# Kernel tuning notes

Hardware: AMD Instinct MI355X
Metric: run time of the kernel (lower is better)

## Reference

```python
import jax, jax.numpy as jnp
import numpy as np

# Fixed genome topology (layered DAG, topologically ordered levels)
B = 4096      # batch
N_IN = 512    # input nodes
H1 = 1536     # hidden level 1
H2 = 1536     # hidden level 2
N_OUT = 512   # output nodes
FAN = 32      # fan-in per non-input node


def setup_inputs() -> dict:
    key = jax.random.key(0)
    ks = jax.random.split(key, 10)
    x = jax.random.normal(ks[0], (B, N_IN), dtype=jnp.float32)
    # level 1: sources among inputs [0, N_IN)
    src0 = jax.random.randint(ks[1], (H1 * FAN,), 0, N_IN, dtype=jnp.int32)
    dst0 = jax.random.randint(ks[2], (H1 * FAN,), 0, H1, dtype=jnp.int32)
    w0 = jax.random.normal(ks[3], (H1 * FAN,), dtype=jnp.float32) * 0.1
    # level 2: sources among inputs + level1 [0, N_IN+H1)
    src1 = jax.random.randint(ks[4], (H2 * FAN,), 0, N_IN + H1, dtype=jnp.int32)
    dst1 = jax.random.randint(ks[5], (H2 * FAN,), 0, H2, dtype=jnp.int32)
    w1 = jax.random.normal(ks[6], (H2 * FAN,), dtype=jnp.float32) * 0.1
    # output level: sources among all earlier nodes [0, N_IN+H1+H2)
    src2 = jax.random.randint(ks[7], (N_OUT * FAN,), 0, N_IN + H1 + H2, dtype=jnp.int32)
    dst2 = jax.random.randint(ks[8], (N_OUT * FAN,), 0, N_OUT, dtype=jnp.int32)
    w2 = jax.random.normal(ks[9], (N_OUT * FAN,), dtype=jnp.float32) * 0.1
    return dict(x=x, src0=src0, dst0=dst0, w0=w0,
                src1=src1, dst1=dst1, w1=w1,
                src2=src2, dst2=dst2, w2=w2)


def _level(node_values, src, dst, w, size):
    # per-edge weighted gather: [B, E]
    vals = node_values[:, src] * w
    # scatter-add into destination nodes of this level: [B, size]
    agg = jnp.zeros((node_values.shape[0], size), node_values.dtype).at[:, dst].add(vals)
    # per-node activation (genome.activation == 'relu'); relu(0)=0 matches
    # original's behavior of leaving unconnected nodes at zero
    return jax.nn.relu(agg)


def reference(x, src0, dst0, w0, src1, dst1, w1, src2, dst2, w2):
    nv = x                                        # [B, N_IN]
    h1 = _level(nv, src0, dst0, w0, H1)           # [B, H1]
    nv = jnp.concatenate([nv, h1], axis=1)        # [B, N_IN+H1]
    h2 = _level(nv, src1, dst1, w1, H2)           # [B, H2]
    nv = jnp.concatenate([nv, h2], axis=1)        # [B, N_IN+H1+H2]
    out = _level(nv, src2, dst2, w2, N_OUT)       # [B, N_OUT]
    return out
```

## Files before the change

### kernel.cpp

```cpp
#include <hip/hip_runtime.h>
#include <hip/hip_fp16.h>
#include <stdint.h>

#define BATCH 4096
#define N_IN  512
#define H1    1536
#define H2    1536
#define N_OUT 512
#define FAN   32
#define E0 (H1 * FAN)
#define E1 (H2 * FAN)
#define E2 (N_OUT * FAN)
#define ETOT (E0 + E1 + E2)
#define NNODES (H1 + H2 + N_OUT)
#define MAXDEG 128

#define OFF_EDGES 33554432
#define OFF_CNT   (OFF_EDGES + NNODES * MAXDEG * 8)

__global__ __launch_bounds__(256) void k_transpose_in(const float* __restrict__ x,
                                                      __half* __restrict__ xT) {
    __shared__ float tile[32][33];
    const int tx = threadIdx.x, ty = threadIdx.y;
    const int n0 = blockIdx.x * 32;
    const int b0 = blockIdx.y * 32;
#pragma unroll
    for (int k = 0; k < 32; k += 8)
        tile[ty + k][tx] = x[(size_t)(b0 + ty + k) * N_IN + (n0 + tx)];
    __syncthreads();
#pragma unroll
    for (int k = 0; k < 32; k += 8)
        xT[(size_t)(n0 + ty + k) * BATCH + (b0 + tx)] = __float2half_rn(tile[tx][ty + k]);
}

__global__ __launch_bounds__(256) void k_fill(const int* __restrict__ s0, const int* __restrict__ d0, const float* __restrict__ w0,
                                              const int* __restrict__ s1, const int* __restrict__ d1, const float* __restrict__ w1,
                                              const int* __restrict__ s2, const int* __restrict__ d2, const float* __restrict__ w2,
                                              int* __restrict__ cnt, int2* __restrict__ edges) {
    const int e = blockIdx.x * 256 + threadIdx.x;
    int src, node; float w;
    if (e < E0)           { src = s0[e];          node = d0[e];                w = w0[e]; }
    else if (e < E0 + E1) { int i = e - E0;       src = s1[i]; node = H1 + d1[i];        w = w1[i]; }
    else                  { int i = e - E0 - E1;  src = s2[i]; node = H1 + H2 + d2[i];   w = w2[i]; }
    const int pos = atomicAdd(&cnt[node], 1);
    if (pos < MAXDEG) edges[node * MAXDEG + pos] = make_int2(src, __float_as_int(w));
}

__global__ __launch_bounds__(256, 8)
void k_level(const int2* __restrict__ edges,
             const int* __restrict__ cnt,
             const uint4* __restrict__ nv,
             uint4* __restrict__ outb) {
    const int lane = threadIdx.x & 63;
    const int wv   = threadIdx.x >> 6;
    const int node = __builtin_amdgcn_readfirstlane((blockIdx.y << 2) | wv);
    const int col8 = (blockIdx.x << 6) | lane;

    int c = cnt[node];
    c = (c < 0) ? 0 : (c > MAXDEG ? MAXDEG : c);

    float a0 = 0.f, a1 = 0.f, a2 = 0.f, a3 = 0.f, a4 = 0.f, a5 = 0.f, a6 = 0.f, a7 = 0.f;

#define ACC8(q, W) {                                                    \
    const __half2 h0 = *(const __half2*)&(q).x;                         \
    const __half2 h1 = *(const __half2*)&(q).y;                         \
    const __half2 h2 = *(const __half2*)&(q).z;                         \
    const __half2 h3 = *(const __half2*)&(q).w;                         \
    a0 = fmaf(__low2float(h0),  (W), a0);                               \
    a1 = fmaf(__high2float(h0), (W), a1);                               \
    a2 = fmaf(__low2float(h1),  (W), a2);                               \
    a3 = fmaf(__high2float(h1), (W), a3);                               \
    a4 = fmaf(__low2float(h2),  (W), a4);                               \
    a5 = fmaf(__high2float(h2), (W), a5);                               \
    a6 = fmaf(__low2float(h3),  (W), a6);                               \
    a7 = fmaf(__high2float(h3), (W), a7); }

    for (int base = 0; base < c; base += 64) {
        const int2 my = edges[(size_t)node * MAXDEG + base + lane];
        const int m = (c - base < 64) ? (c - base) : 64;
        int j = 0;
        for (; j + 4 <= m; j += 4) {
            const int   s0i = __builtin_amdgcn_readlane(my.x, j)     & 4095;
            const int   s1i = __builtin_amdgcn_readlane(my.x, j + 1) & 4095;
            const int   s2i = __builtin_amdgcn_readlane(my.x, j + 2) & 4095;
            const int   s3i = __builtin_amdgcn_readlane(my.x, j + 3) & 4095;
            const float wa  = __int_as_float(__builtin_amdgcn_readlane(my.y, j));
            const float wb  = __int_as_float(__builtin_amdgcn_readlane(my.y, j + 1));
            const float wc  = __int_as_float(__builtin_amdgcn_readlane(my.y, j + 2));
            const float wd  = __int_as_float(__builtin_amdgcn_readlane(my.y, j + 3));
            const uint4 q0 = nv[((size_t)s0i << 9) | col8];
            const uint4 q1 = nv[((size_t)s1i << 9) | col8];
            const uint4 q2 = nv[((size_t)s2i << 9) | col8];
            const uint4 q3 = nv[((size_t)s3i << 9) | col8];
            ACC8(q0, wa);
            ACC8(q1, wb);
            ACC8(q2, wc);
            ACC8(q3, wd);
        }
        for (; j < m; ++j) {
            const int   s0i = __builtin_amdgcn_readlane(my.x, j) & 4095;
            const float wa  = __int_as_float(__builtin_amdgcn_readlane(my.y, j));
            const uint4 q0 = nv[((size_t)s0i << 9) | col8];
            ACC8(q0, wa);
        }
    }
#undef ACC8

    a0 = fmaxf(a0, 0.f); a1 = fmaxf(a1, 0.f); a2 = fmaxf(a2, 0.f); a3 = fmaxf(a3, 0.f);
    a4 = fmaxf(a4, 0.f); a5 = fmaxf(a5, 0.f); a6 = fmaxf(a6, 0.f); a7 = fmaxf(a7, 0.f);

    const __half2 h0 = __floats2half2_rn(a0, a1);
    const __half2 h1 = __floats2half2_rn(a2, a3);
    const __half2 h2 = __floats2half2_rn(a4, a5);
    const __half2 h3 = __floats2half2_rn(a6, a7);
    uint4 p;
    p.x = *(const uint32_t*)&h0; p.y = *(const uint32_t*)&h1;
    p.z = *(const uint32_t*)&h2; p.w = *(const uint32_t*)&h3;
    outb[((size_t)node << 9) | col8] = p;
}

__global__ __launch_bounds__(256) void k_transpose_out(const __half* __restrict__ outh,
                                                       float* __restrict__ out) {
    __shared__ float tile[32][33];
    const int tx = threadIdx.x, ty = threadIdx.y;
    const int n0 = blockIdx.x * 32;
    const int b0 = blockIdx.y * 32;
#pragma unroll
    for (int k = 0; k < 32; k += 8)
        tile[ty + k][tx] = __half2float(outh[(size_t)(n0 + ty + k) * BATCH + (b0 + tx)]);
    __syncthreads();
#pragma unroll
    for (int k = 0; k < 32; k += 8)
        out[(size_t)(b0 + ty + k) * N_OUT + (n0 + tx)] = tile[tx][ty + k];
}

extern "C" void kernel_launch(void* const* d_in, const int* in_sizes, int n_in,
                              void* d_out, int out_size, void* d_ws, size_t ws_size,
                              hipStream_t stream) {
    const float* x  = (const float*)d_in[0];
    const int* s0   = (const int*)d_in[1];
    const int* dd0  = (const int*)d_in[2];
    const float* w0 = (const float*)d_in[3];
    const int* s1   = (const int*)d_in[4];
    const int* dd1  = (const int*)d_in[5];
    const float* w1 = (const float*)d_in[6];
    const int* s2   = (const int*)d_in[7];
    const int* dd2  = (const int*)d_in[8];
    const float* w2 = (const float*)d_in[9];

    char* ws        = (char*)d_ws;
    uint4*    nv4   = (uint4*)ws;
    int2*     edges = (int2*)(ws + OFF_EDGES);
    int*      cnt   = (int*)(ws + OFF_CNT);

    hipMemsetAsync(cnt, 0, NNODES * sizeof(int), stream);
    k_fill<<<ETOT / 256, 256, 0, stream>>>(s0, dd0, w0, s1, dd1, w1, s2, dd2, w2, cnt, edges);

    k_transpose_in<<<dim3(N_IN / 32, BATCH / 32), dim3(32, 8), 0, stream>>>(x, (__half*)ws);

    k_level<<<dim3(8, H1 / 4), 256, 0, stream>>>(edges, cnt, nv4,
                                                 nv4 + (size_t)N_IN * 512);
    k_level<<<dim3(8, H2 / 4), 256, 0, stream>>>(edges + (size_t)H1 * MAXDEG, cnt + H1, nv4,
                                                 nv4 + (size_t)(N_IN + H1) * 512);
    k_level<<<dim3(8, N_OUT / 4), 256, 0, stream>>>(edges + (size_t)(H1 + H2) * MAXDEG, cnt + H1 + H2, nv4,
                                                    nv4 + (size_t)(N_IN + H1 + H2) * 512);

    k_transpose_out<<<dim3(N_OUT / 32, BATCH / 32), dim3(32, 8), 0, stream>>>(
        (const __half*)(ws + (size_t)(N_IN + H1 + H2) * BATCH * 2), (float*)d_out);
}
```

Measured before the change: 147.6 us.

## Split batch columns into two launches per level with 8-byte gathers

Each level kernel now handles 4 fp16 batch columns per lane with uint2 loads instead of 8 with uint4, and is launched twice per level over the two halves of the batch. Each launch touches a smaller slice of node values, so its working set is halved and may fit better in cache, and each thread holds fewer accumulators. In exchange there are twice as many launches, the edge lists and counts are read twice, and per-lane loads are narrower, which can lower achieved memory bandwidth.

```diff
diff --git a/kernel.cpp b/kernel.cpp
--- a/kernel.cpp
+++ b/kernel.cpp
@@ -49,31 +49,26 @@
 __global__ __launch_bounds__(256, 8)
 void k_level(const int2* __restrict__ edges,
              const int* __restrict__ cnt,
-             const uint4* __restrict__ nv,
-             uint4* __restrict__ outb) {
+             const uint2* __restrict__ nv,
+             uint2* __restrict__ outb,
+             const int cb4) {
     const int lane = threadIdx.x & 63;
     const int wv   = threadIdx.x >> 6;
     const int node = __builtin_amdgcn_readfirstlane((blockIdx.y << 2) | wv);
-    const int col8 = (blockIdx.x << 6) | lane;
+    const int col4 = cb4 + (blockIdx.x << 6) + lane;
 
     int c = cnt[node];
     c = (c < 0) ? 0 : (c > MAXDEG ? MAXDEG : c);
 
-    float a0 = 0.f, a1 = 0.f, a2 = 0.f, a3 = 0.f, a4 = 0.f, a5 = 0.f, a6 = 0.f, a7 = 0.f;
+    float a0 = 0.f, a1 = 0.f, a2 = 0.f, a3 = 0.f;
 
-#define ACC8(q, W) {                                                    \
+#define ACC4(q, W) {                                                    \
     const __half2 h0 = *(const __half2*)&(q).x;                         \
     const __half2 h1 = *(const __half2*)&(q).y;                         \
-    const __half2 h2 = *(const __half2*)&(q).z;                         \
-    const __half2 h3 = *(const __half2*)&(q).w;                         \
     a0 = fmaf(__low2float(h0),  (W), a0);                               \
     a1 = fmaf(__high2float(h0), (W), a1);                               \
     a2 = fmaf(__low2float(h1),  (W), a2);                               \
-    a3 = fmaf(__high2float(h1), (W), a3);                               \
-    a4 = fmaf(__low2float(h2),  (W), a4);                               \
-    a5 = fmaf(__high2float(h2), (W), a5);                               \
-    a6 = fmaf(__low2float(h3),  (W), a6);                               \
-    a7 = fmaf(__high2float(h3), (W), a7); }
+    a3 = fmaf(__high2float(h1), (W), a3); }
 
     for (int base = 0; base < c; base += 64) {
         const int2 my = edges[(size_t)node * MAXDEG + base + lane];
@@ -88,35 +83,31 @@
             const float wb  = __int_as_float(__builtin_amdgcn_readlane(my.y, j + 1));
             const float wc  = __int_as_float(__builtin_amdgcn_readlane(my.y, j + 2));
             const float wd  = __int_as_float(__builtin_amdgcn_readlane(my.y, j + 3));
-            const uint4 q0 = nv[((size_t)s0i << 9) | col8];
-            const uint4 q1 = nv[((size_t)s1i << 9) | col8];
-            const uint4 q2 = nv[((size_t)s2i << 9) | col8];
-            const uint4 q3 = nv[((size_t)s3i << 9) | col8];
-            ACC8(q0, wa);
-            ACC8(q1, wb);
-            ACC8(q2, wc);
-            ACC8(q3, wd);
+            const uint2 q0 = nv[((size_t)s0i << 10) | col4];
+            const uint2 q1 = nv[((size_t)s1i << 10) | col4];
+            const uint2 q2 = nv[((size_t)s2i << 10) | col4];
+            const uint2 q3 = nv[((size_t)s3i << 10) | col4];
+            ACC4(q0, wa);
+            ACC4(q1, wb);
+            ACC4(q2, wc);
+            ACC4(q3, wd);
         }
         for (; j < m; ++j) {
             const int   s0i = __builtin_amdgcn_readlane(my.x, j) & 4095;
             const float wa  = __int_as_float(__builtin_amdgcn_readlane(my.y, j));
-            const uint4 q0 = nv[((size_t)s0i << 9) | col8];
-            ACC8(q0, wa);
+            const uint2 q0 = nv[((size_t)s0i << 10) | col4];
+            ACC4(q0, wa);
         }
     }
-#undef ACC8
+#undef ACC4
 
     a0 = fmaxf(a0, 0.f); a1 = fmaxf(a1, 0.f); a2 = fmaxf(a2, 0.f); a3 = fmaxf(a3, 0.f);
-    a4 = fmaxf(a4, 0.f); a5 = fmaxf(a5, 0.f); a6 = fmaxf(a6, 0.f); a7 = fmaxf(a7, 0.f);
 
     const __half2 h0 = __floats2half2_rn(a0, a1);
     const __half2 h1 = __floats2half2_rn(a2, a3);
-    const __half2 h2 = __floats2half2_rn(a4, a5);
-    const __half2 h3 = __floats2half2_rn(a6, a7);
-    uint4 p;
+    uint2 p;
     p.x = *(const uint32_t*)&h0; p.y = *(const uint32_t*)&h1;
-    p.z = *(const uint32_t*)&h2; p.w = *(const uint32_t*)&h3;
-    outb[((size_t)node << 9) | col8] = p;
+    outb[((size_t)node << 10) | col4] = p;
 }
 
 __global__ __launch_bounds__(256) void k_transpose_out(const __half* __restrict__ outh,
@@ -149,7 +140,7 @@
     const float* w2 = (const float*)d_in[9];
 
     char* ws        = (char*)d_ws;
-    uint4*    nv4   = (uint4*)ws;
+    uint2*    nv2   = (uint2*)ws;
     int2*     edges = (int2*)(ws + OFF_EDGES);
     int*      cnt   = (int*)(ws + OFF_CNT);
 
@@ -158,12 +149,18 @@
 
     k_transpose_in<<<dim3(N_IN / 32, BATCH / 32), dim3(32, 8), 0, stream>>>(x, (__half*)ws);
 
-    k_level<<<dim3(8, H1 / 4), 256, 0, stream>>>(edges, cnt, nv4,
-                                                 nv4 + (size_t)N_IN * 512);
-    k_level<<<dim3(8, H2 / 4), 256, 0, stream>>>(edges + (size_t)H1 * MAXDEG, cnt + H1, nv4,
-                                                 nv4 + (size_t)(N_IN + H1) * 512);
-    k_level<<<dim3(8, N_OUT / 4), 256, 0, stream>>>(edges + (size_t)(H1 + H2) * MAXDEG, cnt + H1 + H2, nv4,
-                                                    nv4 + (size_t)(N_IN + H1 + H2) * 512);
+    for (int cb4 = 0; cb4 <= 512; cb4 += 512) {
+        k_level<<<dim3(8, H1 / 4), 256, 0, stream>>>(edges, cnt, nv2,
+                                                     nv2 + (size_t)N_IN * 1024, cb4);
+    }
+    for (int cb4 = 0; cb4 <= 512; cb4 += 512) {
+        k_level<<<dim3(8, H2 / 4), 256, 0, stream>>>(edges + (size_t)H1 * MAXDEG, cnt + H1, nv2,
+                                                     nv2 + (size_t)(N_IN + H1) * 1024, cb4);
+    }
+    for (int cb4 = 0; cb4 <= 512; cb4 += 512) {
+        k_level<<<dim3(8, N_OUT / 4), 256, 0, stream>>>(edges + (size_t)(H1 + H2) * MAXDEG, cnt + H1 + H2, nv2,
+                                                        nv2 + (size_t)(N_IN + H1 + H2) * 1024, cb4);
+    }
 
     k_transpose_out<<<dim3(N_OUT / 32, BATCH / 32), dim3(32, 8), 0, stream>>>(
         (const __half*)(ws + (size_t)(N_IN + H1 + H2) * BATCH * 2), (float*)d_out);
```

Result: slower. 175.5 us (+18.9%).

## Fuse all stages into one cooperative persistent kernel with grid syncs

Applied to the files above, without the earlier changes.

Replaces the memset, edge fill, input transpose, three level kernels and output transpose with a single cooperative kernel of 512 blocks that separates the phases with grid-wide syncs. The goal is to remove the cost of launching multiple kernels and the gaps between them. In exchange, each level is processed by a fixed grid that loops over node groups, so there is less parallelism per level, and every phase boundary now pays for a grid barrier.

```diff
diff --git a/kernel.cpp b/kernel.cpp
--- a/kernel.cpp
+++ b/kernel.cpp
@@ -1,6 +1,9 @@
 #include <hip/hip_runtime.h>
 #include <hip/hip_fp16.h>
+#include <hip/hip_cooperative_groups.h>
 #include <stdint.h>
+
+namespace cg = cooperative_groups;
 
 #define BATCH 4096
 #define N_IN  512
@@ -15,51 +18,29 @@
 #define NNODES (H1 + H2 + N_OUT)
 #define MAXDEG 128
 
+#define NBLK   512
+#define NTHR   256
+#define GSTRIDE (NBLK * NTHR)
+
 #define OFF_EDGES 33554432
 #define OFF_CNT   (OFF_EDGES + NNODES * MAXDEG * 8)
 
-__global__ __launch_bounds__(256) void k_transpose_in(const float* __restrict__ x,
-                                                      __half* __restrict__ xT) {
-    __shared__ float tile[32][33];
-    const int tx = threadIdx.x, ty = threadIdx.y;
-    const int n0 = blockIdx.x * 32;
-    const int b0 = blockIdx.y * 32;
-#pragma unroll
-    for (int k = 0; k < 32; k += 8)
-        tile[ty + k][tx] = x[(size_t)(b0 + ty + k) * N_IN + (n0 + tx)];
-    __syncthreads();
-#pragma unroll
-    for (int k = 0; k < 32; k += 8)
-        xT[(size_t)(n0 + ty + k) * BATCH + (b0 + tx)] = __float2half_rn(tile[tx][ty + k]);
-}
-
-__global__ __launch_bounds__(256) void k_fill(const int* __restrict__ s0, const int* __restrict__ d0, const float* __restrict__ w0,
-                                              const int* __restrict__ s1, const int* __restrict__ d1, const float* __restrict__ w1,
-                                              const int* __restrict__ s2, const int* __restrict__ d2, const float* __restrict__ w2,
-                                              int* __restrict__ cnt, int2* __restrict__ edges) {
-    const int e = blockIdx.x * 256 + threadIdx.x;
-    int src, node; float w;
-    if (e < E0)           { src = s0[e];          node = d0[e];                w = w0[e]; }
-    else if (e < E0 + E1) { int i = e - E0;       src = s1[i]; node = H1 + d1[i];        w = w1[i]; }
-    else                  { int i = e - E0 - E1;  src = s2[i]; node = H1 + H2 + d2[i];   w = w2[i]; }
-    const int pos = atomicAdd(&cnt[node], 1);
-    if (pos < MAXDEG) edges[node * MAXDEG + pos] = make_int2(src, __float_as_int(w));
-}
-
-__global__ __launch_bounds__(256, 8)
-void k_level(const int2* __restrict__ edges,
-             const int* __restrict__ cnt,
-             const uint4* __restrict__ nv,
-             uint4* __restrict__ outb) {
-    const int lane = threadIdx.x & 63;
-    const int wv   = threadIdx.x >> 6;
-    const int node = __builtin_amdgcn_readfirstlane((blockIdx.y << 2) | wv);
-    const int col8 = (blockIdx.x << 6) | lane;
-
-    int c = cnt[node];
-    c = (c < 0) ? 0 : (c > MAXDEG ? MAXDEG : c);
-
-    float a0 = 0.f, a1 = 0.f, a2 = 0.f, a3 = 0.f, a4 = 0.f, a5 = 0.f, a6 = 0.f, a7 = 0.f;
+__device__ __forceinline__ void level_body(const int2* __restrict__ edges,
+                                           const int* __restrict__ cnt,
+                                           const uint4* __restrict__ nv,
+                                           uint4* __restrict__ outb,
+                                           const int H, const int b, const int tid) {
+    const int lane = tid & 63;
+    const int wv   = tid >> 6;
+    const int col8 = ((b & 7) << 6) | lane;
+    const int slot = ((b >> 3) << 2) | wv;
+
+    for (int n0 = 0; n0 < H; n0 += 256) {
+        const int node = __builtin_amdgcn_readfirstlane(n0 + slot);
+        int c = cnt[node];
+        c = (c < 0) ? 0 : (c > MAXDEG ? MAXDEG : c);
+
+        float a0 = 0.f, a1 = 0.f, a2 = 0.f, a3 = 0.f, a4 = 0.f, a5 = 0.f, a6 = 0.f, a7 = 0.f;
 
 #define ACC8(q, W) {                                                    \
     const __half2 h0 = *(const __half2*)&(q).x;                         \
@@ -75,63 +56,122 @@
     a6 = fmaf(__low2float(h3),  (W), a6);                               \
     a7 = fmaf(__high2float(h3), (W), a7); }
 
-    for (int base = 0; base < c; base += 64) {
-        const int2 my = edges[(size_t)node * MAXDEG + base + lane];
-        const int m = (c - base < 64) ? (c - base) : 64;
-        int j = 0;
-        for (; j + 4 <= m; j += 4) {
-            const int   s0i = __builtin_amdgcn_readlane(my.x, j)     & 4095;
-            const int   s1i = __builtin_amdgcn_readlane(my.x, j + 1) & 4095;
-            const int   s2i = __builtin_amdgcn_readlane(my.x, j + 2) & 4095;
-            const int   s3i = __builtin_amdgcn_readlane(my.x, j + 3) & 4095;
-            const float wa  = __int_as_float(__builtin_amdgcn_readlane(my.y, j));
-            const float wb  = __int_as_float(__builtin_amdgcn_readlane(my.y, j + 1));
-            const float wc  = __int_as_float(__builtin_amdgcn_readlane(my.y, j + 2));
-            const float wd  = __int_as_float(__builtin_amdgcn_readlane(my.y, j + 3));
-            const uint4 q0 = nv[((size_t)s0i << 9) | col8];
-            const uint4 q1 = nv[((size_t)s1i << 9) | col8];
-            const uint4 q2 = nv[((size_t)s2i << 9) | col8];
-            const uint4 q3 = nv[((size_t)s3i << 9) | col8];
-            ACC8(q0, wa);
-            ACC8(q1, wb);
-            ACC8(q2, wc);
-            ACC8(q3, wd);
+        for (int base = 0; base < c; base += 64) {
+            const int2 my = edges[(size_t)node * MAXDEG + base + lane];
+            const int m = (c - base < 64) ? (c - base) : 64;
+            int j = 0;
+            for (; j + 4 <= m; j += 4) {
+                const int   s0i = __builtin_amdgcn_readlane(my.x, j)     & 4095;
+                const int   s1i = __builtin_amdgcn_readlane(my.x, j + 1) & 4095;
+                const int   s2i = __builtin_amdgcn_readlane(my.x, j + 2) & 4095;
+                const int   s3i = __builtin_amdgcn_readlane(my.x, j + 3) & 4095;
+                const float wa  = __int_as_float(__builtin_amdgcn_readlane(my.y, j));
+                const float wb  = __int_as_float(__builtin_amdgcn_readlane(my.y, j + 1));
+                const float wc  = __int_as_float(__builtin_amdgcn_readlane(my.y, j + 2));
+                const float wd  = __int_as_float(__builtin_amdgcn_readlane(my.y, j + 3));
+                const uint4 q0 = nv[((size_t)s0i << 9) | col8];
+                const uint4 q1 = nv[((size_t)s1i << 9) | col8];
+                const uint4 q2 = nv[((size_t)s2i << 9) | col8];
+                const uint4 q3 = nv[((size_t)s3i << 9) | col8];
+                ACC8(q0, wa);
+                ACC8(q1, wb);
+                ACC8(q2, wc);
+                ACC8(q3, wd);
+            }
+            for (; j < m; ++j) {
+                const int   s0i = __builtin_amdgcn_readlane(my.x, j) & 4095;
+                const float wa  = __int_as_float(__builtin_amdgcn_readlane(my.y, j));
+                const uint4 q0 = nv[((size_t)s0i << 9) | col8];
+                ACC8(q0, wa);
+            }
         }
-        for (; j < m; ++j) {
-            const int   s0i = __builtin_amdgcn_readlane(my.x, j) & 4095;
-            const float wa  = __int_as_float(__builtin_amdgcn_readlane(my.y, j));
-            const uint4 q0 = nv[((size_t)s0i << 9) | col8];
-            ACC8(q0, wa);
+#undef ACC8
+
+        a0 = fmaxf(a0, 0.f); a1 = fmaxf(a1, 0.f); a2 = fmaxf(a2, 0.f); a3 = fmaxf(a3, 0.f);
+        a4 = fmaxf(a4, 0.f); a5 = fmaxf(a5, 0.f); a6 = fmaxf(a6, 0.f); a7 = fmaxf(a7, 0.f);
+
+        const __half2 h0 = __floats2half2_rn(a0, a1);
+        const __half2 h1 = __floats2half2_rn(a2, a3);
+        const __half2 h2 = __floats2half2_rn(a4, a5);
+        const __half2 h3 = __floats2half2_rn(a6, a7);
+        uint4 p;
+        p.x = *(const uint32_t*)&h0; p.y = *(const uint32_t*)&h1;
+        p.z = *(const uint32_t*)&h2; p.w = *(const uint32_t*)&h3;
+        outb[((size_t)node << 9) | col8] = p;
+    }
+}
+
+__global__ __launch_bounds__(NTHR, 8)
+void k_mega(const float* __restrict__ x,
+            const int* __restrict__ s0, const int* __restrict__ d0, const float* __restrict__ w0,
+            const int* __restrict__ s1, const int* __restrict__ d1, const float* __restrict__ w1,
+            const int* __restrict__ s2, const int* __restrict__ d2, const float* __restrict__ w2,
+            uint4* __restrict__ nv4, int2* __restrict__ edges, int* __restrict__ cnt,
+            float* __restrict__ out) {
+    cg::grid_group grid = cg::this_grid();
+    const int tid = threadIdx.x;
+    const int b   = blockIdx.x;
+
+    __shared__ float tile[32][33];
+
+    for (int i = b * NTHR + tid; i < NNODES; i += GSTRIDE) cnt[i] = 0;
+    grid.sync();
+
+    for (int e = b * NTHR + tid; e < ETOT; e += GSTRIDE) {
+        int src, node; float w;
+        if (e < E0)           { src = s0[e];          node = d0[e];              w = w0[e]; }
+        else if (e < E0 + E1) { int i = e - E0;       src = s1[i]; node = H1 + d1[i];      w = w1[i]; }
+        else                  { int i = e - E0 - E1;  src = s2[i]; node = H1 + H2 + d2[i]; w = w2[i]; }
+        const int pos = atomicAdd(&cnt[node], 1);
+        if (pos < MAXDEG) edges[node * MAXDEG + pos] = make_int2(src, __float_as_int(w));
+    }
+
+    {
+        __half* xT = (__half*)nv4;
+        const int tx = tid & 31, ty = tid >> 5;
+        for (int i = 0; i < 4; ++i) {
+            const int t  = b * 4 + i;
+            const int n0 = (t & 15) << 5;
+            const int b0 = (t >> 4) << 5;
+            __syncthreads();
+#pragma unroll
+            for (int k = 0; k < 32; k += 8)
+                tile[ty + k][tx] = x[(size_t)(b0 + ty + k) * N_IN + (n0 + tx)];
+            __syncthreads();
+#pragma unroll
+            for (int k = 0; k < 32; k += 8)
+                xT[(size_t)(n0 + ty + k) * BATCH + (b0 + tx)] = __float2half_rn(tile[tx][ty + k]);
         }
     }
-#undef ACC8
-
-    a0 = fmaxf(a0, 0.f); a1 = fmaxf(a1, 0.f); a2 = fmaxf(a2, 0.f); a3 = fmaxf(a3, 0.f);
-    a4 = fmaxf(a4, 0.f); a5 = fmaxf(a5, 0.f); a6 = fmaxf(a6, 0.f); a7 = fmaxf(a7, 0.f);
-
-    const __half2 h0 = __floats2half2_rn(a0, a1);
-    const __half2 h1 = __floats2half2_rn(a2, a3);
-    const __half2 h2 = __floats2half2_rn(a4, a5);
-    const __half2 h3 = __floats2half2_rn(a6, a7);
-    uint4 p;
-    p.x = *(const uint32_t*)&h0; p.y = *(const uint32_t*)&h1;
-    p.z = *(const uint32_t*)&h2; p.w = *(const uint32_t*)&h3;
-    outb[((size_t)node << 9) | col8] = p;
-}
-
-__global__ __launch_bounds__(256) void k_transpose_out(const __half* __restrict__ outh,
-                                                       float* __restrict__ out) {
-    __shared__ float tile[32][33];
-    const int tx = threadIdx.x, ty = threadIdx.y;
-    const int n0 = blockIdx.x * 32;
-    const int b0 = blockIdx.y * 32;
-#pragma unroll
-    for (int k = 0; k < 32; k += 8)
-        tile[ty + k][tx] = __half2float(outh[(size_t)(n0 + ty + k) * BATCH + (b0 + tx)]);
-    __syncthreads();
-#pragma unroll
-    for (int k = 0; k < 32; k += 8)
-        out[(size_t)(b0 + ty + k) * N_OUT + (n0 + tx)] = tile[tx][ty + k];
+    grid.sync();
+
+    level_body(edges, cnt, nv4,
+               nv4 + (size_t)N_IN * 512, H1, b, tid);
+    grid.sync();
+    level_body(edges + (size_t)H1 * MAXDEG, cnt + H1, nv4,
+               nv4 + (size_t)(N_IN + H1) * 512, H2, b, tid);
+    grid.sync();
+    level_body(edges + (size_t)(H1 + H2) * MAXDEG, cnt + H1 + H2, nv4,
+               nv4 + (size_t)(N_IN + H1 + H2) * 512, N_OUT, b, tid);
+    grid.sync();
+
+    {
+        const __half* outh = (const __half*)(nv4 + (size_t)(N_IN + H1 + H2) * 512);
+        const int tx = tid & 31, ty = tid >> 5;
+        for (int i = 0; i < 4; ++i) {
+            const int t  = b * 4 + i;
+            const int n0 = (t & 15) << 5;
+            const int b0 = (t >> 4) << 5;
+            __syncthreads();
+#pragma unroll
+            for (int k = 0; k < 32; k += 8)
+                tile[ty + k][tx] = __half2float(outh[(size_t)(n0 + ty + k) * BATCH + (b0 + tx)]);
+            __syncthreads();
+#pragma unroll
+            for (int k = 0; k < 32; k += 8)
+                out[(size_t)(b0 + ty + k) * N_OUT + (n0 + tx)] = tile[tx][ty + k];
+        }
+    }
 }
 
 extern "C" void kernel_launch(void* const* d_in, const int* in_sizes, int n_in,
@@ -152,19 +192,14 @@
     uint4*    nv4   = (uint4*)ws;
     int2*     edges = (int2*)(ws + OFF_EDGES);
     int*      cnt   = (int*)(ws + OFF_CNT);
-
-    hipMemsetAsync(cnt, 0, NNODES * sizeof(int), stream);
-    k_fill<<<ETOT / 256, 256, 0, stream>>>(s0, dd0, w0, s1, dd1, w1, s2, dd2, w2, cnt, edges);
-
-    k_transpose_in<<<dim3(N_IN / 32, BATCH / 32), dim3(32, 8), 0, stream>>>(x, (__half*)ws);
-
-    k_level<<<dim3(8, H1 / 4), 256, 0, stream>>>(edges, cnt, nv4,
-                                                 nv4 + (size_t)N_IN * 512);
-    k_level<<<dim3(8, H2 / 4), 256, 0, stream>>>(edges + (size_t)H1 * MAXDEG, cnt + H1, nv4,
-                                                 nv4 + (size_t)(N_IN + H1) * 512);
-    k_level<<<dim3(8, N_OUT / 4), 256, 0, stream>>>(edges + (size_t)(H1 + H2) * MAXDEG, cnt + H1 + H2, nv4,
-                                                    nv4 + (size_t)(N_IN + H1 + H2) * 512);
-
-    k_transpose_out<<<dim3(N_OUT / 32, BATCH / 32), dim3(32, 8), 0, stream>>>(
-        (const __half*)(ws + (size_t)(N_IN + H1 + H2) * BATCH * 2), (float*)d_out);
+    float*    outp  = (float*)d_out;
+
+    void* args[] = { (void*)&x,
+                     (void*)&s0, (void*)&dd0, (void*)&w0,
+                     (void*)&s1, (void*)&dd1, (void*)&w1,
+                     (void*)&s2, (void*)&dd2, (void*)&w2,
+                     (void*)&nv4, (void*)&edges, (void*)&cnt,
+                     (void*)&outp };
+    hipLaunchCooperativeKernel((const void*)k_mega, dim3(NBLK), dim3(NTHR),
+                               args, 0, stream);
 }
```

New measurement: 480.0 us. +225.1%, slower.

## Replace first sparse level with dense fp16 MFMA GEMM over scattered weight matrix

Applied to the files above, without the earlier changes.

Level one's edges are scattered with half-precision CAS atomics into a dense [H1, N_IN] weight matrix, which a new MFMA kernel multiplies against x. The kernel is double-buffered, loads the weight tiles straight into LDS with global_load_lds, and converts x to fp16 on the fly. This replaces the per-edge gather kernel for the largest level with tensor-core work, since level one reads only 512 inputs. The cost is a dense GEMM with 1536x512 MACs per sample, plus a build kernel whose CAS atomics sum duplicate edges in fp16 and lose some precision.

```diff
diff --git a/kernel.cpp b/kernel.cpp
--- a/kernel.cpp
+++ b/kernel.cpp
@@ -12,11 +12,20 @@
 #define E1 (H2 * FAN)
 #define E2 (N_OUT * FAN)
 #define ETOT (E0 + E1 + E2)
-#define NNODES (H1 + H2 + N_OUT)
 #define MAXDEG 128
-
-#define OFF_EDGES 33554432
-#define OFF_CNT   (OFF_EDGES + NNODES * MAXDEG * 8)
+#define NN_TAB (H2 + N_OUT)
+
+#define OFF_W0  33554432
+#define OFF_CNT (OFF_W0 + 1572864)
+#define OFF_EDG (OFF_CNT + NN_TAB * 4)
+
+typedef _Float16 f16x8 __attribute__((ext_vector_type(8)));
+typedef float    f32x4 __attribute__((ext_vector_type(4)));
+
+#define GLL(SRC, DST)                                                        \
+    __builtin_amdgcn_global_load_lds(                                        \
+        (const __attribute__((address_space(1))) void*)(const void*)(SRC),   \
+        (__attribute__((address_space(3))) void*)(void*)(DST), 16, 0, 0)
 
 __global__ __launch_bounds__(256) void k_transpose_in(const float* __restrict__ x,
                                                       __half* __restrict__ xT) {
@@ -33,17 +42,151 @@
         xT[(size_t)(n0 + ty + k) * BATCH + (b0 + tx)] = __float2half_rn(tile[tx][ty + k]);
 }
 
-__global__ __launch_bounds__(256) void k_fill(const int* __restrict__ s0, const int* __restrict__ d0, const float* __restrict__ w0,
-                                              const int* __restrict__ s1, const int* __restrict__ d1, const float* __restrict__ w1,
-                                              const int* __restrict__ s2, const int* __restrict__ d2, const float* __restrict__ w2,
-                                              int* __restrict__ cnt, int2* __restrict__ edges) {
+__device__ __forceinline__ void atomic_add_half(__half* addr, float val) {
+    uint32_t* base = (uint32_t*)((size_t)addr & ~(size_t)3);
+    const bool hi  = ((size_t)addr & 2) != 0;
+    uint32_t old = *base, assumed;
+    do {
+        assumed = old;
+        __half2 h2 = *(__half2*)&assumed;
+        float f = (hi ? __high2float(h2) : __low2float(h2)) + val;
+        __half2 nh = hi ? __halves2half2(__low2half(h2), __float2half_rn(f))
+                        : __halves2half2(__float2half_rn(f), __high2half(h2));
+        old = atomicCAS(base, assumed, *(uint32_t*)&nh);
+    } while (old != assumed);
+}
+
+__global__ __launch_bounds__(256) void k_build(
+        const int* __restrict__ s0, const int* __restrict__ d0, const float* __restrict__ w0,
+        const int* __restrict__ s1, const int* __restrict__ d1, const float* __restrict__ w1,
+        const int* __restrict__ s2, const int* __restrict__ d2, const float* __restrict__ w2,
+        __half* __restrict__ W0d, int* __restrict__ cnt, int2* __restrict__ edges) {
     const int e = blockIdx.x * 256 + threadIdx.x;
+    if (e < E0) {
+        atomic_add_half(W0d + (size_t)d0[e] * N_IN + s0[e], w0[e]);
+        return;
+    }
     int src, node; float w;
-    if (e < E0)           { src = s0[e];          node = d0[e];                w = w0[e]; }
-    else if (e < E0 + E1) { int i = e - E0;       src = s1[i]; node = H1 + d1[i];        w = w1[i]; }
-    else                  { int i = e - E0 - E1;  src = s2[i]; node = H1 + H2 + d2[i];   w = w2[i]; }
+    if (e < E0 + E1) { const int i = e - E0;      src = s1[i]; node = d1[i];       w = w1[i]; }
+    else             { const int i = e - E0 - E1; src = s2[i]; node = H2 + d2[i];  w = w2[i]; }
     const int pos = atomicAdd(&cnt[node], 1);
     if (pos < MAXDEG) edges[node * MAXDEG + pos] = make_int2(src, __float_as_int(w));
+}
+
+__global__ __launch_bounds__(256, 2)
+void k_gemm1(const __half* __restrict__ W0d,
+             const float* __restrict__ x,
+             __half* __restrict__ nvh) {
+    __shared__ __half lA[2][96 * 64];
+    __shared__ __half lB[2][128 * 64];
+    const int tid  = threadIdx.x;
+    const int lane = tid & 63;
+    const int wv   = tid >> 6;
+    const int wr   = wv >> 1, wc = wv & 1;
+    const int m0   = blockIdx.y * 96;
+    const int n0   = blockIdx.x * 128;
+    const int lrow = lane >> 3;
+    const int lchk = lane & 7;
+    const int brow = tid >> 4;
+    const int bl16 = tid & 15;
+
+    f32x4 acc[3][4] = {};
+    float4 breg[8];
+
+#define ADMA(BUF, KT) {                                                      \
+    _Pragma("unroll")                                                        \
+    for (int it = 0; it < 3; ++it) {                                         \
+        const int row = it * 32 + wv * 8 + lrow;                             \
+        const int sc  = lchk ^ (row & 7);                                    \
+        GLL(W0d + (size_t)(m0 + row) * N_IN + (KT) + sc * 8,                 \
+            lA[BUF] + (it * 32 + wv * 8) * 64);                              \
+    }                                                                        \
+}
+#define BLOAD(KT) {                                                          \
+    _Pragma("unroll")                                                        \
+    for (int it = 0; it < 8; ++it) {                                         \
+        const int r = it * 16 + brow;                                        \
+        breg[it] = *(const float4*)(x + (size_t)(n0 + r) * N_IN + (KT) + bl16 * 4); \
+    }                                                                        \
+}
+#define BWRITE(BUF) {                                                        \
+    _Pragma("unroll")                                                        \
+    for (int it = 0; it < 8; ++it) {                                         \
+        const int r    = it * 16 + brow;                                     \
+        const int byte = r * 128 + (((bl16 >> 1) ^ (r & 7)) * 16) + ((bl16 & 1) * 8); \
+        const __half2 h01 = __floats2half2_rn(breg[it].x, breg[it].y);       \
+        const __half2 h23 = __floats2half2_rn(breg[it].z, breg[it].w);       \
+        uint2 u; u.x = *(const uint32_t*)&h01; u.y = *(const uint32_t*)&h23; \
+        *(uint2*)((char*)&lB[BUF][0] + byte) = u;                            \
+    }                                                                        \
+}
+
+    const int NT = N_IN >> 6;
+    BLOAD(0)
+    ADMA(0, 0)
+    asm volatile("s_waitcnt vmcnt(3)" ::: "memory");
+    __builtin_amdgcn_sched_barrier(0);
+    BWRITE(0)
+
+    int cur = 0;
+    for (int t = 0; t < NT; ++t) {
+        __builtin_amdgcn_s_barrier();
+        __builtin_amdgcn_sched_barrier(0);
+        if (t + 1 < NT) {
+            BLOAD((t + 1) << 6)
+            ADMA(cur ^ 1, (t + 1) << 6)
+            asm volatile("s_waitcnt vmcnt(3)" ::: "memory");
+            __builtin_amdgcn_sched_barrier(0);
+            BWRITE(cur ^ 1)
+        } else {
+            asm volatile("s_waitcnt vmcnt(0)" ::: "memory");
+        }
+        asm volatile("s_waitcnt lgkmcnt(0)" ::: "memory");
+        __builtin_amdgcn_sched_barrier(0);
+        __builtin_amdgcn_s_barrier();
+        __builtin_amdgcn_sched_barrier(0);
+#pragma unroll
+        for (int kk = 0; kk < 2; ++kk) {
+            f16x8 af[3], bf[4];
+#pragma unroll
+            for (int fm = 0; fm < 3; ++fm) {
+                const int row = wr * 48 + fm * 16 + (lane & 15);
+                const int ch  = (kk * 4 + (lane >> 4)) ^ (row & 7);
+                af[fm] = *(const f16x8*)(lA[cur] + row * 64 + ch * 8);
+            }
+#pragma unroll
+            for (int fn = 0; fn < 4; ++fn) {
+                const int row = wc * 64 + fn * 16 + (lane & 15);
+                const int ch  = (kk * 4 + (lane >> 4)) ^ (row & 7);
+                bf[fn] = *(const f16x8*)(lB[cur] + row * 64 + ch * 8);
+            }
+#pragma unroll
+            for (int fm = 0; fm < 3; ++fm)
+#pragma unroll
+                for (int fn = 0; fn < 4; ++fn)
+                    acc[fm][fn] = __builtin_amdgcn_mfma_f32_16x16x32_f16(
+                        af[fm], bf[fn], acc[fm][fn], 0, 0, 0);
+        }
+        cur ^= 1;
+    }
+#undef BWRITE
+#undef BLOAD
+#undef ADMA
+
+    const int cm = (lane >> 4) << 2;
+    const int cn = lane & 15;
+#pragma unroll
+    for (int fm = 0; fm < 3; ++fm)
+#pragma unroll
+        for (int fn = 0; fn < 4; ++fn) {
+            const f32x4 v = acc[fm][fn];
+            const int mm = m0 + wr * 48 + fm * 16 + cm;
+            const int nn = n0 + wc * 64 + fn * 16 + cn;
+#pragma unroll
+            for (int j = 0; j < 4; ++j)
+                nvh[(size_t)(N_IN + mm + j) * BATCH + nn] =
+                    __float2half_rn(fmaxf(v[j], 0.f));
+        }
 }
 
 __global__ __launch_bounds__(256, 8)
@@ -86,7 +229,7 @@
             const int   s3i = __builtin_amdgcn_readlane(my.x, j + 3) & 4095;
             const float wa  = __int_as_float(__builtin_amdgcn_readlane(my.y, j));
             const float wb  = __int_as_float(__builtin_amdgcn_readlane(my.y, j + 1));
-            const float wc  = __int_as_float(__builtin_amdgcn_readlane(my.y, j + 2));
+            const float wc_ = __int_as_float(__builtin_amdgcn_readlane(my.y, j + 2));
             const float wd  = __int_as_float(__builtin_amdgcn_readlane(my.y, j + 3));
             const uint4 q0 = nv[((size_t)s0i << 9) | col8];
             const uint4 q1 = nv[((size_t)s1i << 9) | col8];
@@ -94,7 +237,7 @@
             const uint4 q3 = nv[((size_t)s3i << 9) | col8];
             ACC8(q0, wa);
             ACC8(q1, wb);
-            ACC8(q2, wc);
+            ACC8(q2, wc_);
             ACC8(q3, wd);
         }
         for (; j < m; ++j) {
@@ -148,22 +291,27 @@
     const int* dd2  = (const int*)d_in[8];
     const float* w2 = (const float*)d_in[9];
 
-    char* ws        = (char*)d_ws;
+    char*     ws    = (char*)d_ws;
+    __half*   nvh   = (__half*)ws;
     uint4*    nv4   = (uint4*)ws;
-    int2*     edges = (int2*)(ws + OFF_EDGES);
+    __half*   W0p   = (__half*)(ws + OFF_W0);
     int*      cnt   = (int*)(ws + OFF_CNT);
-
-    hipMemsetAsync(cnt, 0, NNODES * sizeof(int), stream);
-    k_fill<<<ETOT / 256, 256, 0, stream>>>(s0, dd0, w0, s1, dd1, w1, s2, dd2, w2, cnt, edges);
-
-    k_transpose_in<<<dim3(N_IN / 32, BATCH / 32), dim3(32, 8), 0, stream>>>(x, (__half*)ws);
-
-    k_level<<<dim3(8, H1 / 4), 256, 0, stream>>>(edges, cnt, nv4,
-                                                 nv4 + (size_t)N_IN * 512);
-    k_level<<<dim3(8, H2 / 4), 256, 0, stream>>>(edges + (size_t)H1 * MAXDEG, cnt + H1, nv4,
+    int2*     edges = (int2*)(ws + OFF_EDG);
+
+    hipMemsetAsync(W0p, 0, (size_t)1572864 + NN_TAB * 4, stream);
+
+    k_transpose_in<<<dim3(N_IN / 32, BATCH / 32), dim3(32, 8), 0, stream>>>(x, nvh);
+
+    k_build<<<ETOT / 256, 256, 0, stream>>>(s0, dd0, w0, s1, dd1, w1, s2, dd2, w2,
+                                            W0p, cnt, edges);
+
+    k_gemm1<<<dim3(BATCH / 128, H1 / 96), 256, 0, stream>>>(W0p, x, nvh);
+
+    k_level<<<dim3(8, H2 / 4), 256, 0, stream>>>(edges, cnt, nv4,
                                                  nv4 + (size_t)(N_IN + H1) * 512);
-    k_level<<<dim3(8, N_OUT / 4), 256, 0, stream>>>(edges + (size_t)(H1 + H2) * MAXDEG, cnt + H1 + H2, nv4,
-                                                    nv4 + (size_t)(N_IN + H1 + H2) * 512);
+
+    k_level<<<dim3(8, N_OUT / 4), 256, 0, stream>>>(edges + (size_t)H2 * MAXDEG, cnt + H2,
+                                                    nv4, nv4 + (size_t)(N_IN + H1 + H2) * 512);
 
     k_transpose_out<<<dim3(N_OUT / 32, BATCH / 32), dim3(32, 8), 0, stream>>>(
         (const __half*)(ws + (size_t)(N_IN + H1 + H2) * BATCH * 2), (float*)d_out);
```

Result: faster. 143.3 us (-2.9%).
